# Optimization experiments

Hardware: AMD Instinct MI355X
Metric: run time of the kernel (lower is better)

Reference implementation:

```python
import jax, jax.numpy as jnp
import numpy as np

TOP_K = 8
NUM_EXPERTS = 256
N_GROUP = 8
TOPK_GROUP = 4
SCALE = 2.5
RENORMALIZE = True
TOKENS = 131072


def setup_inputs() -> dict:
    key = jax.random.key(0)
    k1, k2 = jax.random.split(key)
    router_logits = jax.random.normal(k1, (TOKENS, NUM_EXPERTS), dtype=jnp.float32)
    expert_bias = jax.random.normal(k2, (NUM_EXPERTS,), dtype=jnp.float32) * 0.1
    return {"router_logits": router_logits, "expert_bias": expert_bias}


def _group_limited_topk(biased):
    # biased: [T, E]
    T = biased.shape[0]
    epg = NUM_EXPERTS // N_GROUP  # experts per group
    grouped = biased.reshape(T, N_GROUP, epg)
    # group score = sum of top-2 expert scores in each group
    top2_vals, _ = jax.lax.top_k(grouped, 2)
    group_scores = top2_vals.sum(axis=-1)  # [T, G]
    _, group_idx = jax.lax.top_k(group_scores, TOPK_GROUP)  # [T, Kg]
    group_mask = jnp.zeros((T, N_GROUP), dtype=bool).at[
        jnp.arange(T)[:, None], group_idx
    ].set(True)
    score_mask = jnp.repeat(group_mask, epg, axis=-1)  # [T, E]
    masked = jnp.where(score_mask, biased, -jnp.inf)
    _, topk_ids = jax.lax.top_k(masked, TOP_K)  # [T, K]
    return topk_ids


def reference(router_logits, expert_bias):
    scores = jax.nn.sigmoid(router_logits.astype(jnp.float32)).astype(router_logits.dtype)
    topk_ids = _group_limited_topk(scores + expert_bias)
    topk_weights = jnp.take_along_axis(scores, topk_ids, axis=-1)  # [T, K]
    if RENORMALIZE and TOP_K > 1:
        topk_weights = topk_weights / (topk_weights.sum(axis=-1, keepdims=True) + 1e-20)
    topk_weights = topk_weights * SCALE
    return topk_weights, topk_ids
```

## Files before the change

### kernel.cpp

```cpp
#include <hip/hip_runtime.h>
#include <math.h>


#define SWZF(x, mask) __int_as_float(__builtin_amdgcn_ds_swizzle(__float_as_int(x), (((mask) << 10) | 0x1F)))
#define SWZI(x, mask) __builtin_amdgcn_ds_swizzle((x), (((mask) << 10) | 0x1F))
#define DPPF(x, ctrl) __int_as_float(__builtin_amdgcn_update_dpp(__float_as_int(x), __float_as_int(x), (ctrl), 0xF, 0xF, true))
#define DPPI(x, ctrl) __builtin_amdgcn_update_dpp((x), (x), (ctrl), 0xF, 0xF, true)
#define QP_X1 0xB1
#define QP_X2 0x4E
#define QP_X3 0x1B

__global__ __launch_bounds__(256) void router_topk_kernel(
    const float* __restrict__ logits,
    const float* __restrict__ bias,
    float* __restrict__ out_w,
    float* __restrict__ out_id,
    int T)
{
    const float NEGINF = -__builtin_inff();
    const int tid  = threadIdx.x;
    const int lane = tid & 63;
    const int wid  = tid >> 6;
    const int s    = tid & 7;
    const int tw   = (tid >> 3) & 7;
    const int token = blockIdx.x * 32 + (tid >> 3);
    const int wtok0 = blockIdx.x * 32 + (wid << 3);

    __shared__ float4 xp[2048];
    float4* xw = xp + (wid << 9);

    {
        float4 g[8];
        #pragma unroll
        for (int j = 0; j < 8; ++j) {
            int r = wtok0 + j;
            r = (r < T) ? r : (T - 1);
            g[j] = ((const float4*)(logits + ((size_t)r << 8)))[lane];
        }
        #pragma unroll
        for (int j = 0; j < 8; ++j)
            xw[(j << 6) | (lane ^ j)] = g[j];
    }

    const float* brw = bias + s * 32;

    float    v[8][4];
    unsigned pix[8];

    #pragma unroll
    for (int c = 0; c < 8; ++c) {
        float4 l = xw[(tw << 6) | (s << 3) | (c ^ tw)];
        float4 b = ((const float4*)brw)[c];
        #pragma unroll
        for (int k = 0; k < 4; ++k) {
            float x = (&l.x)[k];
            v[c][k] = 1.0f / (1.0f + expf(-x)) + (&b.x)[k];
        }
        pix[c] = (unsigned)(s * 32 + c * 4) * 0x01010101u + 0x03020100u;
    }

    float t1 = NEGINF, t2 = NEGINF;
    #pragma unroll
    for (int c = 0; c < 8; ++c) {
        #pragma unroll
        for (int k = 0; k < 4; ++k) {
            float val = v[c][k];
            t2 = __builtin_amdgcn_fmed3f(t1, t2, val);
            t1 = fmaxf(t1, val);
        }
    }
    const float gs = t1 + t2;

    int rank = 0;
    {
        float g1 = DPPF(gs, QP_X1);
        float g2 = DPPF(gs, QP_X2);
        float g3 = DPPF(gs, QP_X3);
        float g4 = SWZF(gs, 4);
        float g5 = DPPF(g4, QP_X1);
        float g6 = DPPF(g4, QP_X2);
        float g7 = DPPF(g4, QP_X3);
        rank += (g1 > gs || (g1 == gs && (s & 1))) ? 1 : 0;
        rank += (g2 > gs || (g2 == gs && (s & 2))) ? 1 : 0;
        rank += (g3 > gs || (g3 == gs && (s & 2))) ? 1 : 0;
        rank += (g4 > gs || (g4 == gs && (s & 4))) ? 1 : 0;
        rank += (g5 > gs || (g5 == gs && (s & 4))) ? 1 : 0;
        rank += (g6 > gs || (g6 == gs && (s & 4))) ? 1 : 0;
        rank += (g7 > gs || (g7 == gs && (s & 4))) ? 1 : 0;
    }
    const bool selected = rank < 4;

    #pragma unroll
    for (int c = 0; c < 8; ++c) {
        #define CE(A, B, KM) { \
            unsigned p  = pix[c]; \
            unsigned ia = (p >> (8*(A))) & 0xFFu; \
            unsigned ib = (p >> (8*(B))) & 0xFFu; \
            bool sw = (v[c][A] < v[c][B]) || (v[c][A] == v[c][B] && ia > ib); \
            float hv = sw ? v[c][B] : v[c][A]; \
            float lv = sw ? v[c][A] : v[c][B]; \
            v[c][A] = hv; v[c][B] = lv; \
            unsigned ps = (p & (KM)) | (ia << (8*(B))) | (ib << (8*(A))); \
            pix[c] = sw ? ps : p; \
        }
        CE(0,1,0xFFFF0000u) CE(2,3,0x0000FFFFu)
        CE(0,2,0xFF00FF00u) CE(1,3,0x00FF00FFu) CE(1,2,0xFF0000FFu)
        #undef CE
    }

    float keepV = 0.0f; int keepI = 0;
    const int sbase8 = s << 3;
    #pragma unroll
    for (int r = 0; r < 8; ++r) {
        #define PICK(av, ai, bv_, bi_, rv, ri) { \
            bool t = ((bv_) > (av)); \
            rv = t ? (bv_) : (av); ri = t ? (bi_) : (ai); }
        float w0v, w1v, w2v, w3v, x0v, x1v, bv;
        int   w0i, w1i, w2i, w3i, x0i, x1i, bi;
        PICK(v[0][0], (int)(pix[0] & 0xFFu), v[1][0], (int)(pix[1] & 0xFFu), w0v, w0i)
        PICK(v[2][0], (int)(pix[2] & 0xFFu), v[3][0], (int)(pix[3] & 0xFFu), w1v, w1i)
        PICK(v[4][0], (int)(pix[4] & 0xFFu), v[5][0], (int)(pix[5] & 0xFFu), w2v, w2i)
        PICK(v[6][0], (int)(pix[6] & 0xFFu), v[7][0], (int)(pix[7] & 0xFFu), w3v, w3i)
        PICK(w0v, w0i, w1v, w1i, x0v, x0i)
        PICK(w2v, w2i, w3v, w3i, x1v, x1i)
        PICK(x0v, x0i, x1v, x1i, bv, bi)
        #undef PICK
        bv = selected ? bv : NEGINF;
        { float ov = DPPF(bv, QP_X1); int oi = DPPI(bi, QP_X1);
          bool t = (ov > bv) || (ov == bv && oi < bi); bv = t ? ov : bv; bi = t ? oi : bi; }
        { float ov = DPPF(bv, QP_X2); int oi = DPPI(bi, QP_X2);
          bool t = (ov > bv) || (ov == bv && oi < bi); bv = t ? ov : bv; bi = t ? oi : bi; }
        { float ov = SWZF(bv, 4);     int oi = SWZI(bi, 4);
          bool t = (ov > bv) || (ov == bv && oi < bi); bv = t ? ov : bv; bi = t ? oi : bi; }
        if (s == r) { keepV = bv; keepI = bi; }
        const int d = (bi >> 2) - sbase8;
        #pragma unroll
        for (int c = 0; c < 8; ++c) {
            bool hit = (d == c);
            v[c][0] = hit ? v[c][1] : v[c][0];
            v[c][1] = hit ? v[c][2] : v[c][1];
            v[c][2] = hit ? v[c][3] : v[c][2];
            v[c][3] = hit ? NEGINF  : v[c][3];
            pix[c]  = hit ? (pix[c] >> 8) : pix[c];
        }
    }

    float w = keepV - bias[keepI];
    float sum = w;
    sum += DPPF(sum, QP_X1);
    sum += DPPF(sum, QP_X2);
    sum += SWZF(sum, 4);
    w = w / (sum + 1e-20f) * 2.5f;

    if (token < T) {
        const size_t o = (size_t)blockIdx.x * 256 + tid;
        out_w[o]  = w;
        out_id[o] = (float)keepI;
    }
}

extern "C" void kernel_launch(void* const* d_in, const int* in_sizes, int n_in,
                              void* d_out, int out_size, void* d_ws, size_t ws_size,
                              hipStream_t stream) {
    const float* logits = (const float*)d_in[0];
    const float* bias   = (const float*)d_in[1];
    const int E = in_sizes[1];
    const int T = in_sizes[0] / E;
    float* out_w  = (float*)d_out;
    float* out_id = out_w + (size_t)T * 8;
    const int blocks = (T + 31) / 32;
    router_topk_kernel<<<blocks, 256, 0, stream>>>(logits, bias, out_w, out_id, T);
}
```

Measured before the change: 208.9 us.

## Redistribute selected groups' experts across lanes to halve per-lane top-k work

After the group ranking, the biased scores are written back to shared memory. Each of the 8 lanes per token then gathers half of one selected group (16 experts), found from a broadcast group bitmask. This replaces each lane holding its own 32 experts, half of which belonged to unselected groups, so the sorting network, per-round argmax and shift-out work drop from 8 chunks to 4. The cost is an extra LDS write/read pass and some mask-decoding instructions.

```diff
diff --git a/kernel.cpp b/kernel.cpp
--- a/kernel.cpp
+++ b/kernel.cpp
@@ -30,22 +30,20 @@
     float4* xw = xp + (wid << 9);
 
     {
-        float4 g[8];
+        float4 gbuf[8];
         #pragma unroll
         for (int j = 0; j < 8; ++j) {
             int r = wtok0 + j;
             r = (r < T) ? r : (T - 1);
-            g[j] = ((const float4*)(logits + ((size_t)r << 8)))[lane];
+            gbuf[j] = ((const float4*)(logits + ((size_t)r << 8)))[lane];
         }
         #pragma unroll
         for (int j = 0; j < 8; ++j)
-            xw[(j << 6) | (lane ^ j)] = g[j];
+            xw[(j << 6) | (lane ^ j)] = gbuf[j];
     }
 
     const float* brw = bias + s * 32;
-
-    float    v[8][4];
-    unsigned pix[8];
+    float v[8][4];
 
     #pragma unroll
     for (int c = 0; c < 8; ++c) {
@@ -56,7 +54,6 @@
             float x = (&l.x)[k];
             v[c][k] = 1.0f / (1.0f + expf(-x)) + (&b.x)[k];
         }
-        pix[c] = (unsigned)(s * 32 + c * 4) * 0x01010101u + 0x03020100u;
     }
 
     float t1 = NEGINF, t2 = NEGINF;
@@ -70,6 +67,10 @@
         }
     }
     const float gs = t1 + t2;
+
+    #pragma unroll
+    for (int c = 0; c < 8; ++c)
+        xw[(tw << 6) | (c << 3) | (s ^ tw)] = make_float4(v[c][0], v[c][1], v[c][2], v[c][3]);
 
     int rank = 0;
     {
@@ -90,16 +91,51 @@
     }
     const bool selected = rank < 4;
 
-    #pragma unroll
-    for (int c = 0; c < 8; ++c) {
+    int msk = selected ? (1 << s) : 0;
+    msk |= DPPI(msk, QP_X1);
+    msk |= DPPI(msk, QP_X2);
+    msk |= SWZI(msk, 4);
+
+    unsigned m0 = (unsigned)msk;
+    int g0 = __builtin_ctz(m0);
+    unsigned m1 = m0 & (m0 - 1);
+    int g1 = __builtin_ctz(m1);
+    unsigned m2 = m1 & (m1 - 1);
+    int g2 = __builtin_ctz(m2);
+    unsigned m3 = m2 & (m2 - 1);
+    int g3 = __builtin_ctz(m3);
+    int ga = (s & 2) ? g1 : g0;
+    int gb = (s & 2) ? g3 : g2;
+    const int grp = (s & 4) ? gb : ga;
+    const int h4  = (s & 1) << 2;
+
+    float    f[4][4];
+    unsigned pix[4];
+    {
+        const int rb = (tw << 6) | (grp ^ tw);
+        #pragma unroll
+        for (int j = 0; j < 4; ++j) {
+            float4 nb = xw[rb | ((h4 + j) << 3)];
+            f[j][0] = nb.x; f[j][1] = nb.y; f[j][2] = nb.z; f[j][3] = nb.w;
+        }
+        const unsigned ebase = (unsigned)(grp * 32 + (h4 << 2));
+        const unsigned pbase = ebase * 0x01010101u;
+        pix[0] = pbase + 0x03020100u;
+        pix[1] = pbase + 0x07060504u;
+        pix[2] = pbase + 0x0B0A0908u;
+        pix[3] = pbase + 0x0F0E0D0Cu;
+    }
+
+    #pragma unroll
+    for (int c = 0; c < 4; ++c) {
         #define CE(A, B, KM) { \
             unsigned p  = pix[c]; \
             unsigned ia = (p >> (8*(A))) & 0xFFu; \
             unsigned ib = (p >> (8*(B))) & 0xFFu; \
-            bool sw = (v[c][A] < v[c][B]) || (v[c][A] == v[c][B] && ia > ib); \
-            float hv = sw ? v[c][B] : v[c][A]; \
-            float lv = sw ? v[c][A] : v[c][B]; \
-            v[c][A] = hv; v[c][B] = lv; \
+            bool sw = (f[c][A] < f[c][B]) || (f[c][A] == f[c][B] && ia > ib); \
+            float hv = sw ? f[c][B] : f[c][A]; \
+            float lv = sw ? f[c][A] : f[c][B]; \
+            f[c][A] = hv; f[c][B] = lv; \
             unsigned ps = (p & (KM)) | (ia << (8*(B))) | (ib << (8*(A))); \
             pix[c] = sw ? ps : p; \
         }
@@ -109,23 +145,16 @@
     }
 
     float keepV = 0.0f; int keepI = 0;
-    const int sbase8 = s << 3;
     #pragma unroll
     for (int r = 0; r < 8; ++r) {
-        #define PICK(av, ai, bv_, bi_, rv, ri) { \
-            bool t = ((bv_) > (av)); \
-            rv = t ? (bv_) : (av); ri = t ? (bi_) : (ai); }
-        float w0v, w1v, w2v, w3v, x0v, x1v, bv;
-        int   w0i, w1i, w2i, w3i, x0i, x1i, bi;
-        PICK(v[0][0], (int)(pix[0] & 0xFFu), v[1][0], (int)(pix[1] & 0xFFu), w0v, w0i)
-        PICK(v[2][0], (int)(pix[2] & 0xFFu), v[3][0], (int)(pix[3] & 0xFFu), w1v, w1i)
-        PICK(v[4][0], (int)(pix[4] & 0xFFu), v[5][0], (int)(pix[5] & 0xFFu), w2v, w2i)
-        PICK(v[6][0], (int)(pix[6] & 0xFFu), v[7][0], (int)(pix[7] & 0xFFu), w3v, w3i)
-        PICK(w0v, w0i, w1v, w1i, x0v, x0i)
-        PICK(w2v, w2i, w3v, w3i, x1v, x1i)
-        PICK(x0v, x0i, x1v, x1i, bv, bi)
-        #undef PICK
-        bv = selected ? bv : NEGINF;
+        const int h0 = (int)(pix[0] & 0xFFu);
+        const int h1 = (int)(pix[1] & 0xFFu);
+        const int h2 = (int)(pix[2] & 0xFFu);
+        const int h3 = (int)(pix[3] & 0xFFu);
+        float w0v, w1v, bv; int w0i, w1i, bi;
+        { bool t = (f[1][0] > f[0][0]); w0v = t ? f[1][0] : f[0][0]; w0i = t ? h1 : h0; }
+        { bool t = (f[3][0] > f[2][0]); w1v = t ? f[3][0] : f[2][0]; w1i = t ? h3 : h2; }
+        { bool t = (w1v > w0v);         bv  = t ? w1v : w0v;         bi  = t ? w1i : w0i; }
         { float ov = DPPF(bv, QP_X1); int oi = DPPI(bi, QP_X1);
           bool t = (ov > bv) || (ov == bv && oi < bi); bv = t ? ov : bv; bi = t ? oi : bi; }
         { float ov = DPPF(bv, QP_X2); int oi = DPPI(bi, QP_X2);
@@ -133,15 +162,37 @@
         { float ov = SWZF(bv, 4);     int oi = SWZI(bi, 4);
           bool t = (ov > bv) || (ov == bv && oi < bi); bv = t ? ov : bv; bi = t ? oi : bi; }
         if (s == r) { keepV = bv; keepI = bi; }
-        const int d = (bi >> 2) - sbase8;
-        #pragma unroll
-        for (int c = 0; c < 8; ++c) {
-            bool hit = (d == c);
-            v[c][0] = hit ? v[c][1] : v[c][0];
-            v[c][1] = hit ? v[c][2] : v[c][1];
-            v[c][2] = hit ? v[c][3] : v[c][2];
-            v[c][3] = hit ? NEGINF  : v[c][3];
-            pix[c]  = hit ? (pix[c] >> 8) : pix[c];
+        {
+            bool hit = (h0 == bi);
+            f[0][0] = hit ? f[0][1] : f[0][0];
+            f[0][1] = hit ? f[0][2] : f[0][1];
+            f[0][2] = hit ? f[0][3] : f[0][2];
+            f[0][3] = hit ? NEGINF  : f[0][3];
+            pix[0]  = hit ? (pix[0] >> 8) : pix[0];
+        }
+        {
+            bool hit = (h1 == bi);
+            f[1][0] = hit ? f[1][1] : f[1][0];
+            f[1][1] = hit ? f[1][2] : f[1][1];
+            f[1][2] = hit ? f[1][3] : f[1][2];
+            f[1][3] = hit ? NEGINF  : f[1][3];
+            pix[1]  = hit ? (pix[1] >> 8) : pix[1];
+        }
+        {
+            bool hit = (h2 == bi);
+            f[2][0] = hit ? f[2][1] : f[2][0];
+            f[2][1] = hit ? f[2][2] : f[2][1];
+            f[2][2] = hit ? f[2][3] : f[2][2];
+            f[2][3] = hit ? NEGINF  : f[2][3];
+            pix[2]  = hit ? (pix[2] >> 8) : pix[2];
+        }
+        {
+            bool hit = (h3 == bi);
+            f[3][0] = hit ? f[3][1] : f[3][0];
+            f[3][1] = hit ? f[3][2] : f[3][1];
+            f[3][2] = hit ? f[3][3] : f[3][2];
+            f[3][3] = hit ? NEGINF  : f[3][3];
+            pix[3]  = hit ? (pix[3] >> 8) : pix[3];
         }
     }
 
```

Measured after the change: 202.0 us. 3.3% less time.
